# Kernel tuning notes

Hardware: AMD Instinct MI355X
Metric: run time of the kernel (lower is better)

Reference implementation:

```python
import jax, jax.numpy as jnp
import numpy as np

H = 32        # query heads
KV = 8        # kv heads
HD = 128      # head_dim
EPS = 1e-6
THETA = 1e6
T = 2048
D = 4096


def _rms_norm(x, w):
    # x: [T, heads, HD]
    var = jnp.mean(jnp.square(x), axis=-1, keepdims=True)
    return x * jax.lax.rsqrt(var + EPS) * w


def _rope(x, cos, sin):
    # NEOX-style rotary: split last dim in halves. x: [T, heads, HD]
    x1, x2 = jnp.split(x, 2, axis=-1)
    return jnp.concatenate([x1 * cos - x2 * sin, x2 * cos + x1 * sin], axis=-1)


def setup_inputs() -> dict:
    key = jax.random.key(0)
    k1, k2, k3 = jax.random.split(key, 3)
    s = 1.0 / np.sqrt(D)
    return {
        "positions": jnp.arange(T, dtype=jnp.int32),
        "hidden_states": jax.random.normal(k1, (T, D), dtype=jnp.float32),
        "w_qkv": jax.random.normal(k2, (D, (H + 2 * KV) * HD), dtype=jnp.float32) * s,
        "q_norm_w": jnp.ones((HD,), dtype=jnp.float32),
        "k_norm_w": jnp.ones((HD,), dtype=jnp.float32),
        "w_o": jax.random.normal(k3, (H * HD, D), dtype=jnp.float32) * s,
    }


def reference(positions, hidden_states, w_qkv, q_norm_w, k_norm_w, w_o):
    scale = HD ** -0.5
    qkv = hidden_states @ w_qkv                              # [T, (H+2KV)*HD]
    q = qkv[:, : H * HD].reshape(T, H, HD)
    k = qkv[:, H * HD : (H + KV) * HD].reshape(T, KV, HD)
    v = qkv[:, (H + KV) * HD :].reshape(T, KV, HD)

    # per-head RMSNorm on q/k (Qwen3 QK-norm)
    q = _rms_norm(q, q_norm_w)
    k = _rms_norm(k, k_norm_w)

    # RoPE
    inv_freq = 1.0 / (THETA ** (jnp.arange(0, HD, 2, dtype=jnp.float32) / HD))
    freqs = positions.astype(jnp.float32)[:, None] * inv_freq  # [T, HD/2]
    cos = jnp.cos(freqs)[:, None, :]                            # [T, 1, HD/2]
    sin = jnp.sin(freqs)[:, None, :]
    q = _rope(q, cos, sin)
    k = _rope(k, cos, sin)

    # GQA: repeat kv heads
    rep = H // KV
    k = jnp.repeat(k, rep, axis=1)                           # [T, H, HD]
    v = jnp.repeat(v, rep, axis=1)

    # causal SDPA
    scores = jnp.einsum("thd,shd->hts", q, k) * scale        # [H, T, T]
    causal = jnp.tril(jnp.ones((T, T), dtype=bool))
    scores = jnp.where(causal[None], scores, jnp.finfo(scores.dtype).min)
    probs = jax.nn.softmax(scores, axis=-1)
    attn = jnp.einsum("hts,shd->thd", probs, v).reshape(T, H * HD)

    return attn @ w_o                                        # [T, D]
```

## Files before the change

### kernel.cpp

```cpp
#include <hip/hip_runtime.h>

#define TT   2048
#define DD   4096
#define NH   32
#define NKVH 8
#define HDM  128
#define KD   4096
#define NQKV 6144

typedef unsigned short u16;
typedef short v8s __attribute__((ext_vector_type(8)));
typedef float v4f __attribute__((ext_vector_type(4)));

#define QSCALE 0.12751744547734565f
#define EOFF   17.312340490667562f

__device__ __forceinline__ u16 f2bf(float f) {
    unsigned u = __builtin_bit_cast(unsigned, f);
    u += 0x7fffu + ((u >> 16) & 1u);
    return (u16)(u >> 16);
}
__device__ __forceinline__ float bf2f(u16 h) {
    return __builtin_bit_cast(float, ((unsigned)h) << 16);
}
__device__ __forceinline__ void gl2lds16(const void* g, void* l) {
    using gv = const __attribute__((address_space(1))) void;
    using lv = __attribute__((address_space(3))) void;
    __builtin_amdgcn_global_load_lds((gv*)g, (lv*)l, 16, 0, 0);
}

__device__ __forceinline__ void transpose_tile64(const float* __restrict__ in,
                                                 u16* __restrict__ out,
                                                 int K, int N, int n0, int k0,
                                                 float* tile, int t) {
    int rc = t >> 4, cc = (t & 15) * 4;
#pragma unroll
    for (int p = 0; p < 4; ++p) {
        int k = p * 16 + rc;
        float4 v = *(const float4*)&in[(size_t)(k0 + k) * N + n0 + cc];
        tile[k * 65 + cc] = v.x; tile[k * 65 + cc + 1] = v.y;
        tile[k * 65 + cc + 2] = v.z; tile[k * 65 + cc + 3] = v.w;
    }
    __syncthreads();
    int rn = t >> 3, ck = (t & 7) * 8;
#pragma unroll
    for (int p = 0; p < 2; ++p) {
        int n = p * 32 + rn;
        v8s tv;
#pragma unroll
        for (int j = 0; j < 8; ++j) tv[j] = (short)f2bf(tile[(ck + j) * 65 + n]);
        *(v8s*)&out[(size_t)(n0 + n) * K + k0 + ck] = tv;
    }
}

__global__ __launch_bounds__(256) void prep_all_kernel(const float* __restrict__ hidden,
                                                       u16* __restrict__ hid_bf,
                                                       const int* __restrict__ positions,
                                                       float* __restrict__ cosT,
                                                       float* __restrict__ sinT,
                                                       const float* __restrict__ w_qkv,
                                                       u16* __restrict__ wqkv_t) {
    __shared__ float tile[64 * 65];
    int b = blockIdx.x;
    if (b < 4096) {
        size_t i = ((size_t)b * 256 + threadIdx.x) * 8;
        float4 a = *(const float4*)&hidden[i];
        float4 c = *(const float4*)&hidden[i + 4];
        v8s tv;
        tv[0] = (short)f2bf(a.x); tv[1] = (short)f2bf(a.y);
        tv[2] = (short)f2bf(a.z); tv[3] = (short)f2bf(a.w);
        tv[4] = (short)f2bf(c.x); tv[5] = (short)f2bf(c.y);
        tv[6] = (short)f2bf(c.z); tv[7] = (short)f2bf(c.w);
        *(v8s*)&hid_bf[i] = tv;
    } else if (b < 4608) {
        int idx = (b - 4096) * 256 + threadIdx.x;
        int tp = idx >> 6, i = idx & 63;
        float invf = exp2f(-(float)i * 0.31143075889569023f);
        float f = (float)positions[tp] * invf;
        cosT[idx] = cosf(f);
        sinT[idx] = sinf(f);
    } else {
        int bx = b - 4608;
        int n0 = (bx % 96) * 64, k0 = (bx / 96) * 64;
        transpose_tile64(w_qkv, wqkv_t, 4096, NQKV, n0, k0, tile, threadIdx.x);
    }
}

template <int MODE>
__global__ __launch_bounds__(256) void gemm_bt_kernel(
    const u16* __restrict__ A, const u16* __restrict__ Bt, float* __restrict__ C, int N,
    const float* __restrict__ qw, const float* __restrict__ kw,
    const float* __restrict__ cosT, const float* __restrict__ sinT,
    u16* __restrict__ Qb, u16* __restrict__ Kb, u16* __restrict__ Vt)
{
    __shared__ __align__(16) u16 smem[16896];
    u16* As = smem;
    u16* Bs = smem + 8192;
    int tid = threadIdx.x;
    int wave = tid >> 6, lane = tid & 63;
    int quad = lane >> 4, l15 = lane & 15;
    int lm = l15 & 7;
    int wm = wave >> 1, wn = wave & 1;
    int m0 = blockIdx.y * 128, n0 = blockIdx.x * 128;

    v4f acc[4][4];
    v4f z4 = {0.f, 0.f, 0.f, 0.f};
#pragma unroll
    for (int mi = 0; mi < 4; ++mi)
#pragma unroll
        for (int ni = 0; ni < 4; ++ni) acc[mi][ni] = z4;

    int rsub = lane >> 3;
    int cg = (lane & 7) ^ rsub;
    const u16* Ag = &A[(size_t)m0 * KD + cg * 8];
    const u16* Bg = &Bt[(size_t)n0 * KD + cg * 8];

    for (int k0 = 0; k0 < KD; k0 += 64) {
        __syncthreads();
#pragma unroll
        for (int c = 0; c < 4; ++c) {
            int ch = wave * 4 + c;
            int row = ch * 8 + rsub;
            gl2lds16(&Ag[(size_t)row * KD + k0], &As[ch * 512]);
            gl2lds16(&Bg[(size_t)row * KD + k0], &Bs[ch * 512]);
        }
        __syncthreads();
#pragma unroll
        for (int ks = 0; ks < 2; ++ks) {
            v8s af[4], bfr[4];
#pragma unroll
            for (int mi = 0; mi < 4; ++mi) {
                int ar = wm * 64 + mi * 16 + l15;
                af[mi] = *(const v8s*)&As[ar * 64 + ((((ks << 2) + quad) ^ lm) << 3)];
            }
#pragma unroll
            for (int ni = 0; ni < 4; ++ni) {
                int br = wn * 64 + ni * 16 + l15;
                bfr[ni] = *(const v8s*)&Bs[br * 64 + ((((ks << 2) + quad) ^ lm) << 3)];
            }
#pragma unroll
            for (int mi = 0; mi < 4; ++mi)
#pragma unroll
                for (int ni = 0; ni < 4; ++ni)
                    acc[mi][ni] = __builtin_amdgcn_mfma_f32_16x16x32_bf16(
                        af[mi], bfr[ni], acc[mi][ni], 0, 0, 0);
        }
    }

    if (MODE == 0) {
#pragma unroll
        for (int mi = 0; mi < 4; ++mi)
#pragma unroll
            for (int ni = 0; ni < 4; ++ni)
#pragma unroll
                for (int r = 0; r < 4; ++r)
                    C[(size_t)(m0 + wm * 64 + mi * 16 + quad * 4 + r) * N +
                      (n0 + wn * 64 + ni * 16 + l15)] = acc[mi][ni][r];
    } else {
        __syncthreads();
        u16* Ct = smem;
#pragma unroll
        for (int mi = 0; mi < 4; ++mi)
#pragma unroll
            for (int ni = 0; ni < 4; ++ni)
#pragma unroll
                for (int r = 0; r < 4; ++r)
                    Ct[(wm * 64 + mi * 16 + quad * 4 + r) * 132 + wn * 64 + ni * 16 + l15] =
                        f2bf(acc[mi][ni][r]);
        __syncthreads();
        int head = blockIdx.x;
        int t0 = blockIdx.y * 128;
        if (head < 40) {
            if (tid < 128) {
                int row = tid;
                const float* w = (head < 32) ? qw : kw;
                float ss = 0.f;
                for (int i = 0; i < 128; ++i) {
                    float x = bf2f(Ct[row * 132 + i]);
                    ss += x * x;
                }
                float rs = rsqrtf(ss * (1.0f / 128.0f) + 1e-6f);
                if (head < 32) rs *= QSCALE;
                int ti = t0 + row;
                for (int i = 0; i < 64; ++i) {
                    float x1 = bf2f(Ct[row * 132 + i]) * rs * w[i];
                    float x2 = bf2f(Ct[row * 132 + 64 + i]) * rs * w[64 + i];
                    float c = cosT[ti * 64 + i], s = sinT[ti * 64 + i];
                    Ct[row * 132 + i]      = f2bf(x1 * c - x2 * s);
                    Ct[row * 132 + 64 + i] = f2bf(x2 * c + x1 * s);
                }
            }
            __syncthreads();
            u16* dst = (head < 32) ? &Qb[((size_t)head * TT + t0) * HDM]
                                   : &Kb[((size_t)(head - 32) * TT + t0) * HDM];
            for (int cix = tid; cix < 128 * 16; cix += 256) {
                int row = cix >> 4, part = (cix & 15) * 8;
                v8s tv;
#pragma unroll
                for (int j = 0; j < 8; ++j) tv[j] = (short)Ct[row * 132 + part + j];
                *(v8s*)&dst[row * HDM + part] = tv;
            }
        } else {
            int kvh = head - 40;
            if (tid < 128) {
                int hd = tid;
#pragma unroll
                for (int tb = 0; tb < 16; ++tb) {
                    v8s tv;
#pragma unroll
                    for (int j = 0; j < 8; ++j) tv[j] = (short)Ct[(tb * 8 + j) * 132 + hd];
                    *(v8s*)&Vt[((size_t)kvh * HDM + hd) * TT + t0 + tb * 8] = tv;
                }
            }
        }
    }
}

__global__ __launch_bounds__(256) void attn_plus_kernel(
    const u16* __restrict__ Qb, const u16* __restrict__ Kb,
    const u16* __restrict__ Vt, u16* __restrict__ Ob,
    const float* __restrict__ w_o, u16* __restrict__ wo_t)
{
    __shared__ __align__(16) char smem_raw[40960];
    int tid = threadIdx.x;
    if (blockIdx.x >= 1024) {
        int bx = blockIdx.x - 1024;
        int n0 = (bx & 63) * 64, k0 = (bx >> 6) * 64;
        transpose_tile64(w_o, wo_t, 4096, 4096, n0, k0, (float*)smem_raw, tid);
        return;
    }
    u16* Kl = (u16*)smem_raw;
    u16* Vl = (u16*)(smem_raw + 16384);
    u16* Pl = (u16*)(smem_raw + 32768);
    int wave = tid >> 6, lane = tid & 63;
    int quad = lane >> 4, l15 = lane & 15;
    int idx = blockIdx.x;
    int h = idx & 31;
    int qb = 31 - (idx >> 5);
    int kv = h >> 2;
    int q0 = qb * 64;
    int lm = l15 & 7;

    v8s qf[4];
    {
        const u16* qr = &Qb[((size_t)h * TT + q0 + wave * 16 + l15) * HDM];
#pragma unroll
        for (int ks = 0; ks < 4; ++ks) qf[ks] = *(const v8s*)&qr[ks * 32 + quad * 8];
    }

    v4f z4 = {0.f, 0.f, 0.f, 0.f};
    v4f of[8];
#pragma unroll
    for (int i = 0; i < 8; ++i) of[i] = z4;
    float lsum[4];
#pragma unroll
    for (int r = 0; r < 4; ++r) lsum[r] = 0.f;
    u16* Pw = &Pl[wave * 1024];

    for (int s0 = 0; s0 <= q0; s0 += 64) {
        __syncthreads();
#pragma unroll
        for (int c = 0; c < 4; ++c) {
            int ch = wave * 4 + c;
            int rk = ch * 4 + (lane >> 4);
            int ck = (lane & 15) ^ (rk & 7);
            gl2lds16(&Kb[((size_t)kv * TT + s0 + rk) * HDM + ck * 8], &Kl[ch * 512]);
            int rv = ch * 8 + (lane >> 3);
            int cv = (lane & 7) ^ (rv & 7);
            gl2lds16(&Vt[((size_t)kv * HDM + rv) * TT + s0 + cv * 8], &Vl[ch * 512]);
        }
        __syncthreads();
        v4f sf[4];
#pragma unroll
        for (int nt = 0; nt < 4; ++nt) {
            v4f cacc = z4;
#pragma unroll
            for (int ks = 0; ks < 4; ++ks)
                cacc = __builtin_amdgcn_mfma_f32_16x16x32_bf16(
                    qf[ks],
                    *(const v8s*)&Kl[(nt * 16 + l15) * 128 + (((ks * 4 + quad) ^ lm) << 3)],
                    cacc, 0, 0, 0);
            sf[nt] = cacc;
        }
        if (s0 == q0) {
#pragma unroll
            for (int nt = 0; nt < 4; ++nt) {
                int sg = s0 + nt * 16 + l15;
#pragma unroll
                for (int r = 0; r < 4; ++r) {
                    int qg = q0 + wave * 16 + quad * 4 + r;
                    if (sg > qg) sf[nt][r] = -3.0e38f;
                }
            }
        }
#pragma unroll
        for (int nt = 0; nt < 4; ++nt)
#pragma unroll
            for (int r = 0; r < 4; ++r) {
                float p = exp2f(sf[nt][r] - EOFF);
                sf[nt][r] = p;
                lsum[r] += p;
            }
#pragma unroll
        for (int nt = 0; nt < 4; ++nt)
#pragma unroll
            for (int r = 0; r < 4; ++r) {
                int row = quad * 4 + r;
                int pch = ((nt << 1) + (l15 >> 3)) ^ (row & 7);
                Pw[row * 64 + pch * 8 + (l15 & 7)] = f2bf(sf[nt][r]);
            }
#pragma unroll
        for (int sub = 0; sub < 2; ++sub) {
            v8s pa = *(const v8s*)&Pw[l15 * 64 + ((((sub << 2) + quad) ^ lm) << 3)];
#pragma unroll
            for (int nt = 0; nt < 8; ++nt)
                of[nt] = __builtin_amdgcn_mfma_f32_16x16x32_bf16(
                    pa,
                    *(const v8s*)&Vl[(nt * 16 + l15) * 64 + ((((sub << 2) + quad) ^ lm) << 3)],
                    of[nt], 0, 0, 0);
        }
    }
#pragma unroll
    for (int off = 1; off < 16; off <<= 1)
#pragma unroll
        for (int r = 0; r < 4; ++r) lsum[r] += __shfl_xor(lsum[r], off, 64);
    float invl[4];
#pragma unroll
    for (int r = 0; r < 4; ++r) invl[r] = 1.0f / lsum[r];
#pragma unroll
    for (int nt = 0; nt < 8; ++nt)
#pragma unroll
        for (int r = 0; r < 4; ++r)
            Ob[(size_t)(q0 + wave * 16 + quad * 4 + r) * (NH * HDM) + h * HDM + nt * 16 + l15] =
                f2bf(of[nt][r] * invl[r]);
}

extern "C" void kernel_launch(void* const* d_in, const int* in_sizes, int n_in,
                              void* d_out, int out_size, void* d_ws, size_t ws_size,
                              hipStream_t stream)
{
    (void)in_sizes; (void)n_in; (void)out_size; (void)ws_size;
    const int*   positions = (const int*)d_in[0];
    const float* hidden    = (const float*)d_in[1];
    const float* w_qkv     = (const float*)d_in[2];
    const float* q_norm_w  = (const float*)d_in[3];
    const float* k_norm_w  = (const float*)d_in[4];
    const float* w_o       = (const float*)d_in[5];
    float* out = (float*)d_out;
    char* ws = (char*)d_ws;
    char* ob = (char*)d_out;

    u16* hid_bf = (u16*)(ws + 0);
    u16* attnO  = (u16*)(ws + 0);
    u16* wqkv_t = (u16*)(ws + (size_t)16777216);
    u16* wo_t   = (u16*)(ws + (size_t)16777216);

    u16*   Qb   = (u16*)(ob + 0);
    u16*   Kb   = (u16*)(ob + (size_t)16777216);
    u16*   Vt   = (u16*)(ob + (size_t)20971520);
    float* cosT = (float*)(ob + (size_t)25165824);
    float* sinT = (float*)(ob + (size_t)25690112);

    prep_all_kernel<<<10752, 256, 0, stream>>>(hidden, hid_bf, positions, cosT, sinT,
                                               w_qkv, wqkv_t);

    gemm_bt_kernel<1><<<dim3(48, 16), 256, 0, stream>>>(
        hid_bf, wqkv_t, nullptr, NQKV, q_norm_w, k_norm_w, cosT, sinT, Qb, Kb, Vt);

    attn_plus_kernel<<<5120, 256, 0, stream>>>(Qb, Kb, Vt, attnO, w_o, wo_t);

    gemm_bt_kernel<0><<<dim3(32, 16), 256, 0, stream>>>(
        attnO, wo_t, out, 4096, nullptr, nullptr, nullptr, nullptr, nullptr, nullptr, nullptr);
}
```

Baseline: 506.4 us.

## Replace QKV GEMM with 256x256 tiled, double-buffered, phase-pipelined kernel

The fused QKV projection moves from 128x128 tiles with 256 threads to 256x256 tiles with 512 threads. It uses a double-buffered LDS (128KB) filled by direct global-to-LDS loads and a four-phase schedule that interleaves loads with MFMA compute, using explicit barriers, waitcnt and setprio. The goal is more data reuse per loaded tile and better overlap of memory with compute. The epilogue now runs the RMSNorm/RoPE/V-transpose path per head half, over 256 rows. The trade-off is a grid of only 192 blocks for 256 CUs, so many CUs sit idle, and the hand-written waitcnt counts are fragile.

Result: faster. 484.4 us (-4.3%).

```diff
diff --git a/kernel.cpp b/kernel.cpp
--- a/kernel.cpp
+++ b/kernel.cpp
@@ -86,12 +86,8 @@
     }
 }
 
-template <int MODE>
 __global__ __launch_bounds__(256) void gemm_bt_kernel(
-    const u16* __restrict__ A, const u16* __restrict__ Bt, float* __restrict__ C, int N,
-    const float* __restrict__ qw, const float* __restrict__ kw,
-    const float* __restrict__ cosT, const float* __restrict__ sinT,
-    u16* __restrict__ Qb, u16* __restrict__ Kb, u16* __restrict__ Vt)
+    const u16* __restrict__ A, const u16* __restrict__ Bt, float* __restrict__ C, int N)
 {
     __shared__ __align__(16) u16 smem[16896];
     u16* As = smem;
@@ -146,33 +142,139 @@
                         af[mi], bfr[ni], acc[mi][ni], 0, 0, 0);
         }
     }
-
-    if (MODE == 0) {
-#pragma unroll
-        for (int mi = 0; mi < 4; ++mi)
-#pragma unroll
-            for (int ni = 0; ni < 4; ++ni)
-#pragma unroll
-                for (int r = 0; r < 4; ++r)
-                    C[(size_t)(m0 + wm * 64 + mi * 16 + quad * 4 + r) * N +
-                      (n0 + wn * 64 + ni * 16 + l15)] = acc[mi][ni][r];
-    } else {
-        __syncthreads();
-        u16* Ct = smem;
-#pragma unroll
-        for (int mi = 0; mi < 4; ++mi)
-#pragma unroll
-            for (int ni = 0; ni < 4; ++ni)
-#pragma unroll
-                for (int r = 0; r < 4; ++r)
-                    Ct[(wm * 64 + mi * 16 + quad * 4 + r) * 132 + wn * 64 + ni * 16 + l15] =
-                        f2bf(acc[mi][ni][r]);
-        __syncthreads();
-        int head = blockIdx.x;
-        int t0 = blockIdx.y * 128;
+#pragma unroll
+    for (int mi = 0; mi < 4; ++mi)
+#pragma unroll
+        for (int ni = 0; ni < 4; ++ni)
+#pragma unroll
+            for (int r = 0; r < 4; ++r)
+                C[(size_t)(m0 + wm * 64 + mi * 16 + quad * 4 + r) * N +
+                  (n0 + wn * 64 + ni * 16 + l15)] = acc[mi][ni][r];
+}
+
+__global__ __launch_bounds__(512, 2) void gemm256_qkv_kernel(
+    const u16* __restrict__ A, const u16* __restrict__ Bt,
+    const float* __restrict__ qw, const float* __restrict__ kw,
+    const float* __restrict__ cosT, const float* __restrict__ sinT,
+    u16* __restrict__ Qb, u16* __restrict__ Kb, u16* __restrict__ Vt)
+{
+    __shared__ __align__(16) char smem_raw[131072];
+    u16* lds = (u16*)smem_raw;
+    const int tid = threadIdx.x;
+    const int wave = tid >> 6, lane = tid & 63;
+    const int quad = lane >> 4, l15 = lane & 15, lm = l15 & 7;
+    const int wm = wave >> 2, wn = wave & 3;
+    const int m0 = blockIdx.y * 256, n0 = blockIdx.x * 256;
+
+    v4f acc[2][2][4][2];
+    v4f z4 = {0.f, 0.f, 0.f, 0.f};
+#pragma unroll
+    for (int a0 = 0; a0 < 2; ++a0)
+#pragma unroll
+        for (int b0 = 0; b0 < 2; ++b0)
+#pragma unroll
+            for (int mi = 0; mi < 4; ++mi)
+#pragma unroll
+                for (int ni = 0; ni < 2; ++ni) acc[a0][b0][mi][ni] = z4;
+
+    const int rsub = lane >> 3;
+    const int cg = (lane & 7) ^ rsub;
+    const u16* Ag = &A[(size_t)m0 * KD + cg * 8];
+    const u16* Bg = &Bt[(size_t)n0 * KD + cg * 8];
+    const int ch0 = wave * 2;
+    const int g0 = (quad ^ lm) << 3;
+    const int g1 = ((4 + quad) ^ lm) << 3;
+
+#define STAGE_A(tt, h) do { \
+    int _b = ((tt) & 1) * 32768; \
+    gl2lds16(&Ag[(size_t)((h) * 128 + (ch0 + 0) * 8 + rsub) * KD + (size_t)(tt) * 64], \
+             &lds[_b + (h) * 8192 + (ch0 + 0) * 512]); \
+    gl2lds16(&Ag[(size_t)((h) * 128 + (ch0 + 1) * 8 + rsub) * KD + (size_t)(tt) * 64], \
+             &lds[_b + (h) * 8192 + (ch0 + 1) * 512]); \
+  } while (0)
+#define STAGE_B(tt, h) do { \
+    int _b = ((tt) & 1) * 32768 + 16384; \
+    gl2lds16(&Bg[(size_t)((h) * 128 + (ch0 + 0) * 8 + rsub) * KD + (size_t)(tt) * 64], \
+             &lds[_b + (h) * 8192 + (ch0 + 0) * 512]); \
+    gl2lds16(&Bg[(size_t)((h) * 128 + (ch0 + 1) * 8 + rsub) * KD + (size_t)(tt) * 64], \
+             &lds[_b + (h) * 8192 + (ch0 + 1) * 512]); \
+  } while (0)
+
+    v8s af[4][2], bfr[2][2];
+
+#define PHASE(QM, QN, RDA, RDB, STAGE_CODE, WAIT_CODE) do { \
+    if (RDA) { \
+      _Pragma("unroll") \
+      for (int mi = 0; mi < 4; ++mi) { \
+        const u16* ap = &lds[bo + ((QM) * 128 + wm * 64 + mi * 16 + l15) * 64]; \
+        af[mi][0] = *(const v8s*)&ap[g0]; \
+        af[mi][1] = *(const v8s*)&ap[g1]; \
+      } } \
+    if (RDB) { \
+      _Pragma("unroll") \
+      for (int ni = 0; ni < 2; ++ni) { \
+        const u16* bp = &lds[bo + 16384 + ((QN) * 128 + wn * 32 + ni * 16 + l15) * 64]; \
+        bfr[ni][0] = *(const v8s*)&bp[g0]; \
+        bfr[ni][1] = *(const v8s*)&bp[g1]; \
+      } } \
+    STAGE_CODE; \
+    __builtin_amdgcn_s_barrier(); \
+    asm volatile("s_waitcnt lgkmcnt(0)" ::: "memory"); \
+    __builtin_amdgcn_sched_barrier(0); \
+    __builtin_amdgcn_s_setprio(1); \
+    _Pragma("unroll") \
+    for (int mi = 0; mi < 4; ++mi) \
+      _Pragma("unroll") \
+      for (int ni = 0; ni < 2; ++ni) { \
+        acc[QM][QN][mi][ni] = __builtin_amdgcn_mfma_f32_16x16x32_bf16( \
+            af[mi][0], bfr[ni][0], acc[QM][QN][mi][ni], 0, 0, 0); \
+        acc[QM][QN][mi][ni] = __builtin_amdgcn_mfma_f32_16x16x32_bf16( \
+            af[mi][1], bfr[ni][1], acc[QM][QN][mi][ni], 0, 0, 0); \
+      } \
+    __builtin_amdgcn_s_setprio(0); \
+    WAIT_CODE; \
+    __builtin_amdgcn_s_barrier(); \
+  } while (0)
+
+    STAGE_A(0, 0); STAGE_B(0, 0); STAGE_B(0, 1); STAGE_A(0, 1);
+    STAGE_A(1, 0); STAGE_B(1, 1); STAGE_A(1, 1);
+    asm volatile("s_waitcnt vmcnt(6)" ::: "memory");
+    __builtin_amdgcn_s_barrier();
+
+#pragma unroll 2
+    for (int t = 0; t < 64; ++t) {
+        const int bo = (t & 1) * 32768;
+        PHASE(0, 0, 1, 1, { if (t + 1 < 64) STAGE_B(t + 1, 0); }, {});
+        PHASE(0, 1, 0, 1, { if (t + 2 < 64) STAGE_A(t + 2, 0); }, {});
+        PHASE(1, 1, 1, 0, { if (t + 2 < 64) STAGE_B(t + 2, 1); }, {});
+        PHASE(1, 0, 0, 1, { if (t + 2 < 64) STAGE_A(t + 2, 1); },
+              { if (t + 2 < 64) { asm volatile("s_waitcnt vmcnt(6)" ::: "memory"); }
+                else            { asm volatile("s_waitcnt vmcnt(0)" ::: "memory"); } });
+    }
+#undef PHASE
+#undef STAGE_A
+#undef STAGE_B
+
+    u16* Ct = lds;
+    const int t0q = blockIdx.y * 256;
+#pragma unroll
+    for (int hh = 0; hh < 2; ++hh) {
+        __syncthreads();
+#pragma unroll
+        for (int qm = 0; qm < 2; ++qm)
+#pragma unroll
+            for (int mi = 0; mi < 4; ++mi)
+#pragma unroll
+                for (int ni = 0; ni < 2; ++ni)
+#pragma unroll
+                    for (int r = 0; r < 4; ++r)
+                        Ct[(qm * 128 + wm * 64 + mi * 16 + quad * 4 + r) * 132 +
+                           wn * 32 + ni * 16 + l15] = f2bf(acc[qm][hh][mi][ni][r]);
+        __syncthreads();
+        const int head = blockIdx.x * 2 + hh;
         if (head < 40) {
-            if (tid < 128) {
-                int row = tid;
+            if (tid < 256) {
+                const int row = tid;
                 const float* w = (head < 32) ? qw : kw;
                 float ss = 0.f;
                 for (int i = 0; i < 128; ++i) {
@@ -181,7 +283,7 @@
                 }
                 float rs = rsqrtf(ss * (1.0f / 128.0f) + 1e-6f);
                 if (head < 32) rs *= QSCALE;
-                int ti = t0 + row;
+                const int ti = t0q + row;
                 for (int i = 0; i < 64; ++i) {
                     float x1 = bf2f(Ct[row * 132 + i]) * rs * w[i];
                     float x2 = bf2f(Ct[row * 132 + 64 + i]) * rs * w[64 + i];
@@ -191,9 +293,9 @@
                 }
             }
             __syncthreads();
-            u16* dst = (head < 32) ? &Qb[((size_t)head * TT + t0) * HDM]
-                                   : &Kb[((size_t)(head - 32) * TT + t0) * HDM];
-            for (int cix = tid; cix < 128 * 16; cix += 256) {
+            u16* dst = (head < 32) ? &Qb[((size_t)head * TT + t0q) * HDM]
+                                   : &Kb[((size_t)(head - 32) * TT + t0q) * HDM];
+            for (int cix = tid; cix < 256 * 16; cix += 512) {
                 int row = cix >> 4, part = (cix & 15) * 8;
                 v8s tv;
 #pragma unroll
@@ -201,15 +303,14 @@
                 *(v8s*)&dst[row * HDM + part] = tv;
             }
         } else {
-            int kvh = head - 40;
+            const int kvh = head - 40;
             if (tid < 128) {
-                int hd = tid;
-#pragma unroll
-                for (int tb = 0; tb < 16; ++tb) {
+                const int hd = tid;
+                for (int tb = 0; tb < 32; ++tb) {
                     v8s tv;
 #pragma unroll
                     for (int j = 0; j < 8; ++j) tv[j] = (short)Ct[(tb * 8 + j) * 132 + hd];
-                    *(v8s*)&Vt[((size_t)kvh * HDM + hd) * TT + t0 + tb * 8] = tv;
+                    *(v8s*)&Vt[((size_t)kvh * HDM + hd) * TT + t0q + tb * 8] = tv;
                 }
             }
         }
@@ -364,11 +465,10 @@
     prep_all_kernel<<<10752, 256, 0, stream>>>(hidden, hid_bf, positions, cosT, sinT,
                                                w_qkv, wqkv_t);
 
-    gemm_bt_kernel<1><<<dim3(48, 16), 256, 0, stream>>>(
-        hid_bf, wqkv_t, nullptr, NQKV, q_norm_w, k_norm_w, cosT, sinT, Qb, Kb, Vt);
+    gemm256_qkv_kernel<<<dim3(24, 8), 512, 0, stream>>>(
+        hid_bf, wqkv_t, q_norm_w, k_norm_w, cosT, sinT, Qb, Kb, Vt);
 
     attn_plus_kernel<<<5120, 256, 0, stream>>>(Qb, Kb, Vt, attnO, w_o, wo_t);
 
-    gemm_bt_kernel<0><<<dim3(32, 16), 256, 0, stream>>>(
-        attnO, wo_t, out, 4096, nullptr, nullptr, nullptr, nullptr, nullptr, nullptr, nullptr);
-}
+    gemm_bt_kernel<<<dim3(32, 16), 256, 0, stream>>>(attnO, wo_t, out, 4096);
+}
```
